# Kernel optimization log

Measured on AMD Instinct MI355X. Metric: run time of the kernel, lower is better.

The kernel has to match this reference:

```python
import jax, jax.numpy as jnp
import numpy as np


def gcn_conv(x, edge_index, W, b):
    # PyG GCNConv with normalize=True: add self-loops, symmetric D^-1/2 A D^-1/2,
    # transform then aggregate messages source->target, then add bias.
    N = x.shape[0]
    row, col = edge_index[0], edge_index[1]  # row: source, col: target
    loop = jnp.arange(N, dtype=edge_index.dtype)
    row = jnp.concatenate([row, loop])
    col = jnp.concatenate([col, loop])
    ones = jnp.ones(row.shape[0], dtype=x.dtype)
    deg = jax.ops.segment_sum(ones, col, num_segments=N)
    dinv = jnp.where(deg > 0, jax.lax.rsqrt(deg), 0.0)
    norm = dinv[row] * dinv[col]            # [E+N]
    h = x @ W                                # [N, d_out] transform first (cheaper aggregation)
    msgs = h[row] * norm[:, None]            # gather + scale
    out = jax.ops.segment_sum(msgs, col, num_segments=N)  # scatter-add to targets
    return out + b


def setup_inputs() -> dict:
    key = jax.random.key(0)
    k = jax.random.split(key, 6)
    N, D, H, C, E = 100000, 256, 32, 2, 3200000
    x = jax.random.normal(k[0], (N, D), dtype=jnp.float32)
    edge_index = jax.random.randint(k[1], (2, E), 0, N, dtype=jnp.int64)
    # glorot-style init for GCN weights
    W1 = jax.random.normal(k[2], (D, H), dtype=jnp.float32) * np.sqrt(2.0 / (D + H))
    b1 = jnp.zeros((H,), dtype=jnp.float32)
    W2 = jax.random.normal(k[3], (H, C), dtype=jnp.float32) * np.sqrt(2.0 / (H + C))
    b2 = jnp.zeros((C,), dtype=jnp.float32)
    return {"x": x, "edge_index": edge_index, "W1": W1, "b1": b1, "W2": W2, "b2": b2}


def reference(x, edge_index, W1, b1, W2, b2):
    # CRD: GCNConv -> relu -> dropout(p=0.5, eval mode -> identity)
    h = jax.nn.relu(gcn_conv(x, edge_index, W1, b1))
    # CLS: GCNConv -> log_softmax over classes
    logits = gcn_conv(h, edge_index, W2, b2)
    return jax.nn.log_softmax(logits, axis=1)
```

## Files before the change

kernel.cpp:

```cpp
#include <hip/hip_runtime.h>
#include <hip/hip_fp16.h>
#include <math.h>

#define DIV_UP(a,b) (((a)+(b)-1)/(b))

typedef _Float16 f16x8 __attribute__((ext_vector_type(8)));
typedef float    f32x4 __attribute__((ext_vector_type(4)));

#define SHIFT 9
#define TPB   (1 << SHIFT)
#define LMASK (TPB - 1)
#define CHUNK 4096

__global__ __launch_bounds__(256) void k_init(int* __restrict__ gcur, int cap,
                                              int* __restrict__ offsets, int N, int E) {
    const int t = threadIdx.x;
    gcur[t] = t * cap;
    if (t == 0) offsets[N] = E;
}

__global__ __launch_bounds__(256) void k_fat(const float* __restrict__ x,
                                             const float* __restrict__ W,
                                             __half* __restrict__ h1,
                                             const int* __restrict__ row,
                                             const int* __restrict__ col,
                                             int* __restrict__ gcur,
                                             unsigned* __restrict__ binned,
                                             int E, int N, int nchunk) {
    __shared__ __align__(16) char smem[24576];
    const int t = threadIdx.x;
    const int bid = blockIdx.x;
    const bool isBin = (bid < 2 * nchunk) && (bid & 1);

    if (!isBin) {
        const int gb = (bid < 2 * nchunk) ? (bid >> 1) : (bid - nchunk);
        _Float16* WlT = (_Float16*)smem;

#pragma unroll
        for (int i = 0; i < 8; ++i) {
            int idx = t + 256 * i;
            float4 v = ((const float4*)W)[idx];
            int k  = idx >> 3;
            int n4 = (idx & 7) * 4;
            int kc = k >> 5, q = (k >> 3) & 3, j = k & 7;
            int ct = n4 >> 4, m0 = n4 & 15;
            _Float16* dst = WlT + ((size_t)((kc * 2 + ct) * 64 + q * 16 + m0) * 8 + j);
            dst[0 * 8] = (_Float16)v.x;
            dst[1 * 8] = (_Float16)v.y;
            dst[2 * 8] = (_Float16)v.z;
            dst[3 * 8] = (_Float16)v.w;
        }
        __syncthreads();

        const int lane = t & 63;
        const int wv   = t >> 6;
        const int m    = lane & 15;
        const int q    = lane >> 4;

        const int rowA   = gb * 64 + wv * 16 + m;
        const int rclamp = min(rowA, N - 1);
        const float* xr  = x + (long long)rclamp * 256 + q * 8;

        f32x4 c0 = {0.f, 0.f, 0.f, 0.f}, c1 = {0.f, 0.f, 0.f, 0.f};
#pragma unroll
        for (int kc = 0; kc < 8; ++kc) {
            float4 v0 = *(const float4*)(xr + kc * 32);
            float4 v1 = *(const float4*)(xr + kc * 32 + 4);
            f16x8 b0 = *(const f16x8*)&WlT[(size_t)((kc * 2 + 0) * 64 + lane) * 8];
            f16x8 b1 = *(const f16x8*)&WlT[(size_t)((kc * 2 + 1) * 64 + lane) * 8];
            f16x8 a;
            a[0] = (_Float16)v0.x; a[1] = (_Float16)v0.y;
            a[2] = (_Float16)v0.z; a[3] = (_Float16)v0.w;
            a[4] = (_Float16)v1.x; a[5] = (_Float16)v1.y;
            a[6] = (_Float16)v1.z; a[7] = (_Float16)v1.w;
            c0 = __builtin_amdgcn_mfma_f32_16x16x32_f16(a, b0, c0, 0, 0, 0);
            c1 = __builtin_amdgcn_mfma_f32_16x16x32_f16(a, b1, c1, 0, 0, 0);
        }

        const int orow = gb * 64 + wv * 16 + q * 4;
#pragma unroll
        for (int r = 0; r < 4; ++r) {
            int gr = orow + r;
            if (gr < N) {
                h1[gr * 32 + m]      = __float2half(c0[r]);
                h1[gr * 32 + 16 + m] = __float2half(c1[r]);
            }
        }
    } else {
        int* hist  = (int*)smem;
        int* loff  = hist + 256;
        int* gbase = loff + 256;
        int* lcur  = gbase + 256;
        unsigned* staged     = (unsigned*)(smem + 4096);
        unsigned char* binOf = (unsigned char*)(smem + 4096 + 16384);

        const int base = (bid >> 1) * CHUNK;
        const int n = min(CHUNK, E - base);

        hist[t] = 0;
        __syncthreads();

        unsigned pk[CHUNK / 256];
        int bn[CHUNK / 256];
#pragma unroll
        for (int k = 0; k < CHUNK / 256; ++k) {
            int i = base + t + k * 256;
            if (i < E) {
                int c = col[i], r = row[i];
                bn[k] = c >> SHIFT;
                pk[k] = ((unsigned)r << SHIFT) | (unsigned)(c & LMASK);
                atomicAdd(&hist[bn[k]], 1);
            } else bn[k] = -1;
        }
        __syncthreads();

        int v = hist[t];
        loff[t] = v;
        __syncthreads();
#pragma unroll
        for (int off = 1; off < 256; off <<= 1) {
            int y = (t >= off) ? loff[t - off] : 0;
            __syncthreads();
            loff[t] += y;
            __syncthreads();
        }
        int excl = loff[t] - v;
        gbase[t] = v ? atomicAdd(&gcur[t], v) : 0;
        lcur[t]  = excl;
        __syncthreads();
        loff[t] = excl;
        __syncthreads();

#pragma unroll
        for (int k = 0; k < CHUNK / 256; ++k) {
            if (bn[k] >= 0) {
                int p = atomicAdd(&lcur[bn[k]], 1);
                staged[p] = pk[k];
                binOf[p] = (unsigned char)bn[k];
            }
        }
        __syncthreads();

        for (int i = t; i < n; i += 256) {
            int b = binOf[i];
            binned[gbase[b] + (i - loff[b])] = staged[i];
        }
    }
}

__global__ __launch_bounds__(512) void k_csr2(const unsigned* __restrict__ binned,
                                              const int* __restrict__ gcur, int cap,
                                              int* __restrict__ offsets,
                                              float* __restrict__ dinv,
                                              int* __restrict__ srcs,
                                              __half* __restrict__ h1, int N) {
    __shared__ int h[TPB];
    __shared__ int cur[TPB];
    __shared__ int rbuf[512];
    const int t = threadIdx.x, b = blockIdx.x;
    const int beg = b * cap, end = gcur[b];

    rbuf[t] = (t < 256 && t < b) ? (gcur[t] - t * cap) : 0;
    h[t] = 0;
    __syncthreads();
#pragma unroll
    for (int off = 256; off > 0; off >>= 1) {
        if (t < off) rbuf[t] += rbuf[t + off];
        __syncthreads();
    }
    const int obase = rbuf[0];

    for (int i = beg + t; i < end; i += 512)
        atomicAdd(&h[binned[i] & LMASK], 1);
    __syncthreads();

    int cnt = h[t];
#pragma unroll
    for (int off = 1; off < 512; off <<= 1) {
        int y = (t >= off) ? h[t - off] : 0;
        __syncthreads();
        h[t] += y;
        __syncthreads();
    }
    int excl = h[t] - cnt;
    int g = (b << SHIFT) + t;
    int pos0 = obase + excl;
    float di = 0.f;
    if (g < N) {
        offsets[g] = pos0;
        di = rsqrtf((float)(1 + cnt));
        dinv[g] = di;
    }
    cur[t] = pos0;
    __syncthreads();

    for (int i = beg + t; i < end; i += 512) {
        unsigned v = binned[i];
        int pos = atomicAdd(&cur[v & LMASK], 1);
        srcs[pos] = (int)(v >> SHIFT);
    }

    if (g < N) {
        uint4* hp4 = (uint4*)(h1 + (size_t)g * 32);
#pragma unroll
        for (int k4 = 0; k4 < 4; ++k4) {
            uint4 v = hp4[k4];
            __half2* ph = (__half2*)&v;
#pragma unroll
            for (int k2 = 0; k2 < 4; ++k2) {
                float2 u = __half22float2(ph[k2]);
                ph[k2] = __floats2half2_rn(u.x * di, u.y * di);
            }
            hp4[k4] = v;
        }
    }
}

__global__ void k_agg1(const int* __restrict__ offsets, const int* __restrict__ srcs,
                       const float* __restrict__ dinv, const __half* __restrict__ h1w,
                       const float* __restrict__ b1, const float* __restrict__ W2,
                       __half2* __restrict__ tw, int N) {
    long long g = (long long)blockIdx.x * blockDim.x + threadIdx.x;
    int node = (int)(g >> 5), f = (int)(g & 31);
    if (node >= N) return;
    const int sub = f >> 2, q = f & 3;
    const int beg = offsets[node], end = offsets[node + 1];
    const uint4* h4 = (const uint4*)h1w;

    float a0 = 0.f, a1 = 0.f, a2 = 0.f, a3 = 0.f;
    float a4 = 0.f, a5 = 0.f, a6 = 0.f, a7 = 0.f;

    for (int j = beg; j < end; j += 16) {
        int e0 = j + sub, e1 = j + 8 + sub;
        int s0 = srcs[min(e0, end - 1)];
        int s1 = srcs[min(e1, end - 1)];
        float m0 = (e0 < end) ? 1.f : 0.f;
        float m1 = (e1 < end) ? 1.f : 0.f;
        uint4 rv0 = h4[s0 * 4 + q];
        uint4 rv1 = h4[s1 * 4 + q];
        __half2 p; float2 u;
        p = *(__half2*)&rv0.x; u = __half22float2(p); a0 = fmaf(u.x, m0, a0); a1 = fmaf(u.y, m0, a1);
        p = *(__half2*)&rv0.y; u = __half22float2(p); a2 = fmaf(u.x, m0, a2); a3 = fmaf(u.y, m0, a3);
        p = *(__half2*)&rv0.z; u = __half22float2(p); a4 = fmaf(u.x, m0, a4); a5 = fmaf(u.y, m0, a5);
        p = *(__half2*)&rv0.w; u = __half22float2(p); a6 = fmaf(u.x, m0, a6); a7 = fmaf(u.y, m0, a7);
        p = *(__half2*)&rv1.x; u = __half22float2(p); a0 = fmaf(u.x, m1, a0); a1 = fmaf(u.y, m1, a1);
        p = *(__half2*)&rv1.y; u = __half22float2(p); a2 = fmaf(u.x, m1, a2); a3 = fmaf(u.y, m1, a3);
        p = *(__half2*)&rv1.z; u = __half22float2(p); a4 = fmaf(u.x, m1, a4); a5 = fmaf(u.y, m1, a5);
        p = *(__half2*)&rv1.w; u = __half22float2(p); a6 = fmaf(u.x, m1, a6); a7 = fmaf(u.y, m1, a7);
    }
#pragma unroll
    for (int s = 4; s < 32; s <<= 1) {
        a0 += __shfl_xor(a0, s, 32); a1 += __shfl_xor(a1, s, 32);
        a2 += __shfl_xor(a2, s, 32); a3 += __shfl_xor(a3, s, 32);
        a4 += __shfl_xor(a4, s, 32); a5 += __shfl_xor(a5, s, 32);
        a6 += __shfl_xor(a6, s, 32); a7 += __shfl_xor(a7, s, 32);
    }
    if (sub == 0) {
        float di = dinv[node];
        uint4 rv = h4[node * 4 + q];
        float sf[8];
        {
            __half2 p; float2 u;
            p = *(__half2*)&rv.x; u = __half22float2(p); sf[0] = u.x; sf[1] = u.y;
            p = *(__half2*)&rv.y; u = __half22float2(p); sf[2] = u.x; sf[3] = u.y;
            p = *(__half2*)&rv.z; u = __half22float2(p); sf[4] = u.x; sf[5] = u.y;
            p = *(__half2*)&rv.w; u = __half22float2(p); sf[6] = u.x; sf[7] = u.y;
        }
        float av[8] = {a0, a1, a2, a3, a4, a5, a6, a7};
        float t0 = 0.f, t1 = 0.f;
#pragma unroll
        for (int k = 0; k < 8; ++k) {
            int feat = q * 8 + k;
            float hv = fmaf(di, av[k] + sf[k], b1[feat]);
            hv = fmaxf(hv, 0.f);
            t0 = fmaf(hv, W2[feat * 2 + 0], t0);
            t1 = fmaf(hv, W2[feat * 2 + 1], t1);
        }
        t0 += __shfl_xor(t0, 1, 32); t0 += __shfl_xor(t0, 2, 32);
        t1 += __shfl_xor(t1, 1, 32); t1 += __shfl_xor(t1, 2, 32);
        if (q == 0) tw[node] = __floats2half2_rn(di * t0, di * t1);
    }
}

__global__ void k_agg2(const int* __restrict__ offsets, const int* __restrict__ srcs,
                       const float* __restrict__ dinv, const __half2* __restrict__ tw,
                       const float* __restrict__ b2, float* __restrict__ out, int N) {
    long long g = (long long)blockIdx.x * blockDim.x + threadIdx.x;
    int node = (int)(g >> 4), f = (int)(g & 15);
    if (node >= N) return;
    int beg = offsets[node], end = offsets[node + 1];
    float a0 = 0.f, a1 = 0.f;
    for (int j = beg + f; j < end; j += 16) {
        int s = srcs[j];
        float2 u = __half22float2(tw[s]);
        a0 += u.x;
        a1 += u.y;
    }
#pragma unroll
    for (int s = 8; s; s >>= 1) {
        a0 += __shfl_xor(a0, s, 64);
        a1 += __shfl_xor(a1, s, 64);
    }
    if (f == 0) {
        float di = dinv[node];
        float2 u = __half22float2(tw[node]);
        float z0 = di * (a0 + u.x) + b2[0];
        float z1 = di * (a1 + u.y) + b2[1];
        float m = fmaxf(z0, z1);
        float lse = m + logf(expf(z0 - m) + expf(z1 - m));
        ((float2*)out)[node] = float2{z0 - lse, z1 - lse};
    }
}

extern "C" void kernel_launch(void* const* d_in, const int* in_sizes, int n_in,
                              void* d_out, int out_size, void* d_ws, size_t ws_size,
                              hipStream_t stream) {
    const float* x  = (const float*)d_in[0];
    const int*   ei = (const int*)d_in[1];
    const float* W1 = (const float*)d_in[2];
    const float* b1 = (const float*)d_in[3];
    const float* W2 = (const float*)d_in[4];
    const float* b2 = (const float*)d_in[5];

    const int H = in_sizes[3];
    const int D = in_sizes[2] / H;
    const int N = in_sizes[0] / D;
    const int E = in_sizes[1] / 2;
    (void)H; (void)n_in; (void)out_size; (void)ws_size;

    const int* row = ei;
    const int* col = ei + E;

    const int K_used = ((N - 1) >> SHIFT) + 1;
    const int cap    = (DIV_UP(E, K_used) * 5 / 4 + 255) & ~255;
    const int nchunk = DIV_UP(E, CHUNK);
    const int gemmB  = DIV_UP(N, 64);

    char* p = (char*)d_ws;
    auto alloc = [&](size_t bytes) { char* q = p; p += (bytes + 255) & ~(size_t)255; return q; };
    int*      offsets = (int*)     alloc((size_t)(N + 1) * 4);
    int*      gcur    = (int*)     alloc(256 * 4);
    float*    dinv    = (float*)   alloc((size_t)N * 4);
    unsigned* binned  = (unsigned*)alloc((size_t)K_used * cap * 4);
    __half*   h1      = (__half*)  alloc((size_t)N * 32 * 2);
    int*      srcs    = (int*)     alloc((size_t)E * 4);
    __half2*  tw      = (__half2*) alloc((size_t)N * 4);

    k_init <<<1, 256, 0, stream>>>(gcur, cap, offsets, N, E);
    k_fat  <<<gemmB + nchunk, 256, 0, stream>>>(x, W1, h1, row, col, gcur, binned, E, N, nchunk);
    k_csr2 <<<K_used, 512, 0, stream>>>(binned, gcur, cap, offsets, dinv, srcs, h1, N);
    k_agg1 <<<(int)DIV_UP((long long)N * 32, 256), 256, 0, stream>>>(offsets, srcs, dinv, h1, b1, W2, tw, N);
    k_agg2 <<<(int)DIV_UP((long long)N * 16, 256), 256, 0, stream>>>(offsets, srcs, dinv, tw, b2, (float*)d_out, N);
}
```

Before: 282.5 us.

## Use wave-shuffle scans, 1024-thread CSR build, and binned-edge second-layer aggregation

Replaces the shared-memory Hillis-Steele prefix scans, which need a barrier at every step, in the binning and CSR kernels with wave-level shuffle scans plus a small cross-wave fixup. The CSR kernel now runs 1024 threads per bin and splits the per-node h1 rescale across two threads. The second-layer aggregation no longer walks the CSR per node. Instead each bin block reads its binned edges directly and accumulates into LDS with float atomics, which adds LDS atomic contention and makes the summation order nondeterministic.

New measurement: 303.8 us. 1.08x slower.

```diff
diff --git a/kernel.cpp b/kernel.cpp
--- a/kernel.cpp
+++ b/kernel.cpp
@@ -27,7 +27,7 @@
                                              int* __restrict__ gcur,
                                              unsigned* __restrict__ binned,
                                              int E, int N, int nchunk) {
-    __shared__ __align__(16) char smem[24576];
+    __shared__ __align__(16) char smem[24608];
     const int t = threadIdx.x;
     const int bid = blockIdx.x;
     const bool isBin = (bid < 2 * nchunk) && (bid & 1);
@@ -93,6 +93,7 @@
         int* lcur  = gbase + 256;
         unsigned* staged     = (unsigned*)(smem + 4096);
         unsigned char* binOf = (unsigned char*)(smem + 4096 + 16384);
+        int* wtot            = (int*)(smem + 4096 + 16384 + 4096);
 
         const int base = (bid >> 1) * CHUNK;
         const int n = min(CHUNK, E - base);
@@ -114,20 +115,21 @@
         }
         __syncthreads();
 
-        int v = hist[t];
-        loff[t] = v;
-        __syncthreads();
-#pragma unroll
-        for (int off = 1; off < 256; off <<= 1) {
-            int y = (t >= off) ? loff[t - off] : 0;
-            __syncthreads();
-            loff[t] += y;
-            __syncthreads();
-        }
-        int excl = loff[t] - v;
-        gbase[t] = v ? atomicAdd(&gcur[t], v) : 0;
-        lcur[t]  = excl;
-        __syncthreads();
+        const int hv = hist[t];
+        int sc = hv;
+#pragma unroll
+        for (int s = 1; s < 64; s <<= 1) {
+            int y = __shfl_up(sc, s, 64);
+            if ((t & 63) >= s) sc += y;
+        }
+        if ((t & 63) == 63) wtot[t >> 6] = sc;
+        __syncthreads();
+        int woff = 0;
+#pragma unroll
+        for (int j = 0; j < 3; ++j) if (j < (t >> 6)) woff += wtot[j];
+        const int excl = sc + woff - hv;
+        gbase[t] = hv ? atomicAdd(&gcur[t], hv) : 0;
+        lcur[t] = excl;
         loff[t] = excl;
         __syncthreads();
 
@@ -142,68 +144,76 @@
         __syncthreads();
 
         for (int i = t; i < n; i += 256) {
-            int b = binOf[i];
-            binned[gbase[b] + (i - loff[b])] = staged[i];
-        }
-    }
-}
-
-__global__ __launch_bounds__(512) void k_csr2(const unsigned* __restrict__ binned,
-                                              const int* __restrict__ gcur, int cap,
-                                              int* __restrict__ offsets,
-                                              float* __restrict__ dinv,
-                                              int* __restrict__ srcs,
-                                              __half* __restrict__ h1, int N) {
+            int bb = binOf[i];
+            binned[gbase[bb] + (i - loff[bb])] = staged[i];
+        }
+    }
+}
+
+__global__ __launch_bounds__(1024) void k_csr2(const unsigned* __restrict__ binned,
+                                               const int* __restrict__ gcur, int cap,
+                                               int* __restrict__ offsets,
+                                               float* __restrict__ dinv,
+                                               int* __restrict__ srcs,
+                                               __half* __restrict__ h1, int N) {
     __shared__ int h[TPB];
     __shared__ int cur[TPB];
-    __shared__ int rbuf[512];
+    __shared__ float sdi[TPB];
+    __shared__ int wred[16];
     const int t = threadIdx.x, b = blockIdx.x;
+    const int lane = t & 63, wv = t >> 6;
     const int beg = b * cap, end = gcur[b];
 
-    rbuf[t] = (t < 256 && t < b) ? (gcur[t] - t * cap) : 0;
-    h[t] = 0;
-    __syncthreads();
-#pragma unroll
-    for (int off = 256; off > 0; off >>= 1) {
-        if (t < off) rbuf[t] += rbuf[t + off];
-        __syncthreads();
-    }
-    const int obase = rbuf[0];
-
-    for (int i = beg + t; i < end; i += 512)
+    int contrib = (t < 256 && t < b) ? (gcur[t] - t * cap) : 0;
+#pragma unroll
+    for (int s = 1; s < 64; s <<= 1) contrib += __shfl_xor(contrib, s, 64);
+    if (t < TPB) h[t] = 0;
+    if (lane == 0 && wv < 4) wred[wv] = contrib;
+    __syncthreads();
+    const int obase = wred[0] + wred[1] + wred[2] + wred[3];
+
+    for (int i = beg + t; i < end; i += 1024)
         atomicAdd(&h[binned[i] & LMASK], 1);
     __syncthreads();
 
-    int cnt = h[t];
-#pragma unroll
-    for (int off = 1; off < 512; off <<= 1) {
-        int y = (t >= off) ? h[t - off] : 0;
-        __syncthreads();
-        h[t] += y;
-        __syncthreads();
-    }
-    int excl = h[t] - cnt;
-    int g = (b << SHIFT) + t;
-    int pos0 = obase + excl;
-    float di = 0.f;
-    if (g < N) {
-        offsets[g] = pos0;
-        di = rsqrtf((float)(1 + cnt));
-        dinv[g] = di;
-    }
-    cur[t] = pos0;
-    __syncthreads();
-
-    for (int i = beg + t; i < end; i += 512) {
+    const int cnt = (t < TPB) ? h[t] : 0;
+    int sc = cnt;
+#pragma unroll
+    for (int s = 1; s < 64; s <<= 1) {
+        int y = __shfl_up(sc, s, 64);
+        if (lane >= s) sc += y;
+    }
+    if (t < TPB && lane == 63) wred[8 + wv] = sc;
+    __syncthreads();
+    if (t < TPB) {
+        int woff = 0;
+        for (int j = 0; j < wv; ++j) woff += wred[8 + j];
+        const int excl = sc + woff - cnt;
+        const int g = (b << SHIFT) + t;
+        const int pos0 = obase + excl;
+        float di = 0.f;
+        if (g < N) {
+            offsets[g] = pos0;
+            di = rsqrtf((float)(1 + cnt));
+            dinv[g] = di;
+        }
+        cur[t] = pos0;
+        sdi[t] = di;
+    }
+    __syncthreads();
+
+    for (int i = beg + t; i < end; i += 1024) {
         unsigned v = binned[i];
         int pos = atomicAdd(&cur[v & LMASK], 1);
         srcs[pos] = (int)(v >> SHIFT);
     }
 
-    if (g < N) {
-        uint4* hp4 = (uint4*)(h1 + (size_t)g * 32);
-#pragma unroll
-        for (int k4 = 0; k4 < 4; ++k4) {
+    const int node = (b << SHIFT) + (t >> 1);
+    if (node < N) {
+        float di = sdi[t >> 1];
+        uint4* hp4 = (uint4*)(h1 + (size_t)node * 32) + (t & 1) * 2;
+#pragma unroll
+        for (int k4 = 0; k4 < 2; ++k4) {
             uint4 v = hp4[k4];
             __half2* ph = (__half2*)&v;
 #pragma unroll
@@ -282,33 +292,36 @@
     }
 }
 
-__global__ void k_agg2(const int* __restrict__ offsets, const int* __restrict__ srcs,
-                       const float* __restrict__ dinv, const __half2* __restrict__ tw,
-                       const float* __restrict__ b2, float* __restrict__ out, int N) {
-    long long g = (long long)blockIdx.x * blockDim.x + threadIdx.x;
-    int node = (int)(g >> 4), f = (int)(g & 15);
-    if (node >= N) return;
-    int beg = offsets[node], end = offsets[node + 1];
-    float a0 = 0.f, a1 = 0.f;
-    for (int j = beg + f; j < end; j += 16) {
-        int s = srcs[j];
-        float2 u = __half22float2(tw[s]);
-        a0 += u.x;
-        a1 += u.y;
-    }
-#pragma unroll
-    for (int s = 8; s; s >>= 1) {
-        a0 += __shfl_xor(a0, s, 64);
-        a1 += __shfl_xor(a1, s, 64);
-    }
-    if (f == 0) {
-        float di = dinv[node];
-        float2 u = __half22float2(tw[node]);
-        float z0 = di * (a0 + u.x) + b2[0];
-        float z1 = di * (a1 + u.y) + b2[1];
-        float m = fmaxf(z0, z1);
-        float lse = m + logf(expf(z0 - m) + expf(z1 - m));
-        ((float2*)out)[node] = float2{z0 - lse, z1 - lse};
+__global__ __launch_bounds__(1024) void k_cls(const unsigned* __restrict__ binned,
+                                              const int* __restrict__ gcur, int cap,
+                                              const float* __restrict__ dinv,
+                                              const __half2* __restrict__ tw,
+                                              const float* __restrict__ b2,
+                                              float* __restrict__ out, int N) {
+    __shared__ float lacc[2 * TPB];
+    const int t = threadIdx.x, b = blockIdx.x;
+    lacc[t] = 0.f;
+    __syncthreads();
+    const int beg = b * cap, end = gcur[b];
+    for (int i = beg + t; i < end; i += 1024) {
+        unsigned v = binned[i];
+        int loc = v & LMASK;
+        float2 u = __half22float2(tw[v >> SHIFT]);
+        atomicAdd(&lacc[2 * loc],     u.x);
+        atomicAdd(&lacc[2 * loc + 1], u.y);
+    }
+    __syncthreads();
+    if (t < TPB) {
+        int g = (b << SHIFT) + t;
+        if (g < N) {
+            float di = dinv[g];
+            float2 u = __half22float2(tw[g]);
+            float z0 = di * (lacc[2 * t]     + u.x) + b2[0];
+            float z1 = di * (lacc[2 * t + 1] + u.y) + b2[1];
+            float m = fmaxf(z0, z1);
+            float lse = m + logf(expf(z0 - m) + expf(z1 - m));
+            ((float2*)out)[g] = float2{z0 - lse, z1 - lse};
+        }
     }
 }
 
@@ -348,7 +361,7 @@
 
     k_init <<<1, 256, 0, stream>>>(gcur, cap, offsets, N, E);
     k_fat  <<<gemmB + nchunk, 256, 0, stream>>>(x, W1, h1, row, col, gcur, binned, E, N, nchunk);
-    k_csr2 <<<K_used, 512, 0, stream>>>(binned, gcur, cap, offsets, dinv, srcs, h1, N);
+    k_csr2 <<<K_used, 1024, 0, stream>>>(binned, gcur, cap, offsets, dinv, srcs, h1, N);
     k_agg1 <<<(int)DIV_UP((long long)N * 32, 256), 256, 0, stream>>>(offsets, srcs, dinv, h1, b1, W2, tw, N);
-    k_agg2 <<<(int)DIV_UP((long long)N * 16, 256), 256, 0, stream>>>(offsets, srcs, dinv, tw, b2, (float*)d_out, N);
-}
+    k_cls  <<<K_used, 1024, 0, stream>>>(binned, gcur, cap, dinv, tw, b2, (float*)d_out, N);
+}
```
